# Kernel tuning notes

Hardware: AMD Instinct MI355X
Metric: run time of the kernel (lower is better)

The kernel has to match this reference:

```python
import jax, jax.numpy as jnp
import numpy as np

B, W, G, E, NI, K = 2048, 8192, 8, 128, 16, 15


def setup_inputs() -> dict:
    key = jax.random.key(0)
    ks = jax.random.split(key, 12)
    wavelengths_nm = jnp.linspace(300.0, 400.0, W, dtype=jnp.float32)
    # Rayleigh optical depth (Hansen & Travis style approximation), AMF=1 column
    lam_um = wavelengths_nm / 1000.0
    rayleigh_od = (0.008569 * lam_um ** -4
                   * (1.0 + 0.0113 * lam_um ** -2 + 0.00013 * lam_um ** -4)).astype(jnp.float32)
    return {
        "gas_columns": jax.random.uniform(ks[0], (B, G), jnp.float32),
        "instrument_ids": jax.random.randint(ks[1], (B,), 0, NI),
        "nuisance_latent": jax.random.normal(ks[2], (B, G), jnp.float32),
        "air_mass": 1.0 + 2.0 * jax.random.uniform(ks[3], (B,), jnp.float32),
        "wavelengths_nm": wavelengths_nm,
        "absorption": 0.1 * jax.random.uniform(ks[4], (G, W), jnp.float32),
        "continuum_basis": 0.05 * jax.random.normal(ks[5], (G + 1, W), jnp.float32),
        "rayleigh_od": rayleigh_od,
        "embed_table": jax.random.normal(ks[6], (NI, E), jnp.float32),
        "w1": jax.random.normal(ks[7], (E + G, 64), jnp.float32) / np.sqrt(E + G),
        "b1": jnp.zeros((64,), jnp.float32),
        "w2": jax.random.normal(ks[8], (64, 7), jnp.float32) / 8.0,
        "b2": jnp.zeros((7,), jnp.float32),
    }


def _gaussian_kernel(width_px, kernel_size):
    half = (kernel_size - 1) / 2
    pos = jnp.linspace(-half, half, kernel_size, dtype=width_px.dtype)  # [K]
    k = jnp.exp(-0.5 * (pos[None, :] / (width_px[:, None] + 1e-6)) ** 2)  # [B,K]
    return k / k.sum(axis=1, keepdims=True)


def _forward(gas_columns, nuisance_latent, air_mass, wavelengths_nm, absorption,
             continuum_basis, rayleigh_od, embed_table, w1, b1, w2, b2,
             instrument_ids):
    b = gas_columns.shape[0]
    am = air_mass[:, None]                                   # [B,1]
    scaled = gas_columns * am                                # [B,G]
    optical_depth = scaled @ absorption                      # [B,W]
    ones = jnp.ones((b, 1), gas_columns.dtype)
    continuum = jnp.concatenate([gas_columns, ones], axis=1) @ continuum_basis  # [B,W]
    differential = optical_depth + continuum + am * rayleigh_od[None, :]

    # nuisance MLP on [latent, embedding]
    embed = embed_table[instrument_ids]                      # [B,E]
    nin = jnp.concatenate([nuisance_latent, embed], axis=-1)
    h = jax.nn.gelu(nin @ w1 + b1, approximate=False)
    p = h @ w2 + b2                                          # [B,7]

    gain = jax.nn.softplus(p[:, 0]) + 0.001
    offset = p[:, 1]
    woff = 0.05 * jnp.tanh(p[:, 2])
    wscale = 1.0 + 0.005 * jnp.tanh(p[:, 3])
    lsf = jnp.clip(jax.nn.softplus(p[:, 4]) + 0.001, 0.2, 5.0)
    stray = jax.nn.sigmoid(p[:, 5]) * 0.05
    nonlin = 0.02 * jnp.tanh(p[:, 6])

    # per-sample wavelength shift/scale + linear resampling
    new_wl = wavelengths_nm[None, :] * wscale[:, None] + woff[:, None]  # [B,W]
    differential = jax.vmap(lambda wq, d: jnp.interp(wq, wavelengths_nm, d))(new_wl, differential)

    # per-sample Gaussian LSF convolution (replicate padding)
    kernel = _gaussian_kernel(lsf, K)                        # [B,K]
    pad = K // 2
    padded = jnp.pad(differential, ((0, 0), (pad, pad)), mode='edge')  # [B,W+K-1]
    n = differential.shape[1]
    convolved = sum(padded[:, k:k + n] * kernel[:, k:k + 1] for k in range(K))

    counts = jnp.exp(-convolved)
    post = gain[:, None] * counts + offset[:, None]
    total_nl = jnp.clip(nonlin, -0.04, 0.04)                 # instrument nonlinearity = 0
    nl_counts = post + total_nl[:, None] * post ** 2
    total_stray = jnp.clip(stray, 0.0, 0.2)                  # instrument stray = 0
    simulated = (1.0 - total_stray[:, None]) * nl_counts \
        + total_stray[:, None] * nl_counts.mean(axis=1, keepdims=True)
    return simulated


def reference(gas_columns, instrument_ids, nuisance_latent, air_mass,
              wavelengths_nm, absorption, continuum_basis, rayleigh_od,
              embed_table, w1, b1, w2, b2):
    return _forward(gas_columns, nuisance_latent, air_mass, wavelengths_nm,
                    absorption, continuum_basis, rayleigh_od, embed_table,
                    w1, b1, w2, b2, instrument_ids)
```

## Files before the change

### kernel.cpp

```cpp
#include <hip/hip_runtime.h>

#define W_ 8192
#define NBATCH 2048
#define TB 4
#define NT 512
#define CCH 1024
#define NCH 8
#define NSUB 16
#define RING 2048
#define RSTR 2052
#define IRW 1040

typedef unsigned short u16_t;
typedef _Float16 h2v __attribute__((ext_vector_type(2)));

__device__ __forceinline__ u16_t f2h(float x){ _Float16 h=(_Float16)x; return __builtin_bit_cast(u16_t,h); }
__device__ __forceinline__ float h2f(u16_t u){ return (float)__builtin_bit_cast(_Float16,u); }
__device__ __forceinline__ unsigned pk2(float a,float b){ return (unsigned)f2h(a)|((unsigned)f2h(b)<<16); }
__device__ __forceinline__ float dot2u(unsigned a,unsigned b,float c){
#if __has_builtin(__builtin_amdgcn_fdot2)
  return __builtin_amdgcn_fdot2(__builtin_bit_cast(h2v,a),__builtin_bit_cast(h2v,b),c,false);
#else
  h2v ha=__builtin_bit_cast(h2v,a), hb=__builtin_bit_cast(h2v,b);
  return c+(float)ha[0]*(float)hb[0]+(float)ha[1]*(float)hb[1];
#endif
}
__device__ __forceinline__ unsigned pkrtz(float a,float b){
#if __has_builtin(__builtin_amdgcn_cvt_pkrtz)
  return __builtin_bit_cast(unsigned, __builtin_amdgcn_cvt_pkrtz(a,b));
#else
  return pk2(a,b);
#endif
}
__device__ __forceinline__ float softplusf(float x){ return fmaxf(x,0.f)+log1pf(expf(-fabsf(x))); }

__global__ void doas_pack(const float* __restrict__ absn, const float* __restrict__ cbn,
                          const float* __restrict__ ray, unsigned* __restrict__ Tp){
  int w = blockIdx.x*256 + threadIdx.x;
  if (w >= W_) return;
  #pragma unroll
  for (int q=0;q<4;++q) Tp[q*W_+w]     = pk2(absn[(2*q)*W_+w], absn[(2*q+1)*W_+w]);
  #pragma unroll
  for (int q=0;q<4;++q) Tp[(4+q)*W_+w] = pk2(cbn[(2*q)*W_+w],  cbn[(2*q+1)*W_+w]);
  Tp[8*W_+w] = pk2(cbn[8*W_+w], ray[w]);
}

template<int PACKED>
__global__ __launch_bounds__(NT, 4)
void doas_main(const float* __restrict__ gas, const int* __restrict__ iid,
               const float* __restrict__ nuis, const float* __restrict__ air,
               const float* __restrict__ wl, const float* __restrict__ absn,
               const float* __restrict__ cbn, const float* __restrict__ ray,
               const float* __restrict__ emb, const float* __restrict__ w1,
               const float* __restrict__ b1, const float* __restrict__ w2,
               const float* __restrict__ b2, const unsigned* __restrict__ Tp,
               float* __restrict__ out)
{
  extern __shared__ char smem[];
  float* ringF = (float*)smem;
  float* irowS = (float*)(smem + TB*RSTR*4);
  float* hS    = (float*)(smem + TB*RSTR*4 + TB*IRW*4);
  float* pS    = hS + TB*64;
  float* scalS = pS + TB*8;
  float* wsumS = scalS + TB*32;

  const int tid = threadIdx.x;
  const int r0 = blockIdx.x * TB;

  if (tid < TB*64) {
    int rr = tid >> 6, j = tid & 63;
    int id = iid[r0 + rr];
    float acc = b1[j];
    const float* nrow = nuis + (size_t)(r0 + rr) * 8;
    #pragma unroll
    for (int i = 0; i < 8; ++i) acc = fmaf(nrow[i], w1[i*64 + j], acc);
    const float* erow = emb + (size_t)id * 128;
    for (int i = 0; i < 128; ++i) acc = fmaf(erow[i], w1[(8+i)*64 + j], acc);
    hS[rr*64 + j] = 0.5f * acc * (1.0f + erff(acc * 0.70710678118654752f));
  }
  __syncthreads();
  if (tid < TB*7) {
    int rr = tid / 7, k = tid % 7;
    float p = b2[k];
    for (int j = 0; j < 64; ++j) p = fmaf(hS[rr*64+j], w2[j*7+k], p);
    pS[rr*8+k] = p;
  }
  __syncthreads();
  if (tid < TB) {
    int rr = tid;
    float p0=pS[rr*8+0], p1=pS[rr*8+1], p2=pS[rr*8+2], p3=pS[rr*8+3],
          p4=pS[rr*8+4], p5=pS[rr*8+5], p6=pS[rr*8+6];
    float gainv = softplusf(p0) + 0.001f;
    float offv  = p1;
    float woffv = 0.05f * tanhf(p2);
    float wscv  = 1.0f + 0.005f * tanhf(p3);
    float lsf   = fminf(fmaxf(softplusf(p4) + 0.001f, 0.2f), 5.0f);
    float strv  = (1.0f/(1.0f+expf(-p5))) * 0.05f;
    float nlin  = 0.02f * tanhf(p6);
    nlin = fminf(fmaxf(nlin, -0.04f), 0.04f);
    strv = fminf(fmaxf(strv, 0.0f), 0.2f);
    float iw = 1.0f/(lsf + 1e-6f);
    float ks[15]; float ksum = 0.f;
    #pragma unroll
    for (int k2=0;k2<15;++k2){ float pp=(float)(k2-7)*iw; float e=expf(-0.5f*pp*pp); ks[k2]=e; ksum+=e; }
    float inv = 1.0f/ksum;
    float* sc = scalS + rr*32;
    #pragma unroll
    for (int k2=0;k2<15;++k2) sc[k2]=ks[k2]*inv;
    sc[15]=wscv; sc[16]=woffv; sc[17]=gainv; sc[18]=offv; sc[19]=nlin; sc[20]=strv;
    sc[22]=air[r0+rr];
    #pragma unroll
    for (int g=0; g<8; ++g) sc[23+g] = gas[(size_t)(r0+rr)*8+g];
  }
  __syncthreads();

  unsigned csg[TB][9];
  #pragma unroll
  for (int rr=0; rr<TB; ++rr){
    const float* scr = scalS + rr*32;
    float amr = scr[22];
    #pragma unroll
    for (int q=0;q<4;++q)
      csg[rr][q] = (unsigned)__builtin_amdgcn_readfirstlane(
          (int)pk2(scr[23+2*q]*amr, scr[23+2*q+1]*amr));
    #pragma unroll
    for (int q=0;q<4;++q)
      csg[rr][4+q] = (unsigned)__builtin_amdgcn_readfirstlane(
          (int)pk2(scr[23+2*q], scr[23+2*q+1]));
    csg[rr][8] = (unsigned)__builtin_amdgcn_readfirstlane((int)pk2(1.0f, amr));
  }

  const int r  = tid >> 7;
  const int wi = tid & 127;
  const float* sc = scalS + r*32;
  float kw[15];
  #pragma unroll
  for (int k2=0;k2<15;++k2) kw[k2]=sc[k2];
  const float wscale = sc[15], woff = sc[16], gainv = sc[17], offv = sc[18], nlin = sc[19];
  const float posoff = (300.0f*(wscale - 1.0f) + woff) * (8191.0f/100.0f);

  float* ring = ringF + r*RSTR;
  float* irow = irowS + r*IRW;

  auto do_diff = [&](int s){
    const int e = s*NT + tid;
    float a0=0.f, a1=0.f, a2=0.f, a3=0.f;
    if (PACKED){
      #pragma unroll
      for (int q=0;q<9;++q){
        unsigned d = Tp[q*W_ + e];
        a0 = dot2u(d, csg[0][q], a0);
        a1 = dot2u(d, csg[1][q], a1);
        a2 = dot2u(d, csg[2][q], a2);
        a3 = dot2u(d, csg[3][q], a3);
      }
    } else {
      float av[9][2];
      #pragma unroll
      for (int q=0;q<4;++q){ av[q][0]=absn[(2*q)*W_+e]; av[q][1]=absn[(2*q+1)*W_+e]; }
      #pragma unroll
      for (int q=0;q<4;++q){ av[4+q][0]=cbn[(2*q)*W_+e]; av[4+q][1]=cbn[(2*q+1)*W_+e]; }
      av[8][0]=cbn[8*W_+e]; av[8][1]=ray[e];
      float acc[TB]={0.f,0.f,0.f,0.f};
      #pragma unroll
      for (int rr=0;rr<TB;++rr){
        #pragma unroll
        for (int q=0;q<9;++q){
          acc[rr] = fmaf(h2f((u16_t)(csg[rr][q]&0xffffu)), av[q][0], acc[rr]);
          acc[rr] = fmaf(h2f((u16_t)(csg[rr][q]>>16)),     av[q][1], acc[rr]);
        }
      }
      a0=acc[0]; a1=acc[1]; a2=acc[2]; a3=acc[3];
    }
    const int p = e & (RING-1);
    ringF[0*RSTR+p]=a0; ringF[1*RSTR+p]=a1; ringF[2*RSTR+p]=a2; ringF[3*RSTR+p]=a3;
    if (p == 0){
      ringF[0*RSTR+RING]=a0; ringF[1*RSTR+RING]=a1;
      ringF[2*RSTR+RING]=a2; ringF[3*RSTR+RING]=a3;
    }
  };

  do_diff(0); do_diff(1); do_diff(2);

  float accsum = 0.f;
  unsigned nlp[NCH][4];

  #pragma unroll
  for (int c = 0; c < NCH; ++c) {
    const int cs = c * CCH;
    const bool eLo = (c == 0), eHi = (c == NCH-1);
    if (c >= 1) {
      if (2*c+1 < NSUB) do_diff(2*c+1);
      if (2*c+2 < NSUB) do_diff(2*c+2);
    }
    __syncthreads();
    #pragma unroll
    for (int it = 0; it < 5; ++it) {
      int jj = it*256 + 2*wi;
      if (jj < CCH + 14) {
        float v2[2];
        #pragma unroll
        for (int u=0; u<2; ++u){
          int j = cs - 7 + jj + u;
          int jc = j;
          if (eLo) jc = max(jc, 0);
          if (eHi) jc = min(jc, W_-1);
          float pos = fmaf((float)jc, wscale, posoff);
          if (eLo) pos = fmaxf(pos, 0.0f);
          if (eHi) pos = fminf(pos, 8191.0f);
          int i0 = (int)pos;
          if (eHi) i0 = min(i0, W_-2);
          float fr = pos - (float)i0;
          int p = i0 & (RING-1);
          float d0 = ring[p], d1 = ring[p+1];
          v2[u] = fmaf(fr, d1-d0, d0);
        }
        *(float2*)(irow + jj) = make_float2(v2[0], v2[1]);
      }
    }
    __syncthreads();
    {
      const int b0 = 8*wi;
      const float4* qp = (const float4*)(irow + b0);
      float4 A=qp[0], B=qp[1], C=qp[2], D=qp[3], E=qp[4], F=qp[5];
      float wr[24] = {A.x,A.y,A.z,A.w, B.x,B.y,B.z,B.w, C.x,C.y,C.z,C.w,
                      D.x,D.y,D.z,D.w, E.x,E.y,E.z,E.w, F.x,F.y,F.z,F.w};
      float nlv[8];
      #pragma unroll
      for (int j=0;j<8;++j){
        float cv = 0.f;
        #pragma unroll
        for (int t=0;t<15;++t) cv = fmaf(wr[j+t], kw[t], cv);
        float counts = __expf(-cv);
        float post = fmaf(gainv, counts, offv);
        float v = fmaf(nlin*post, post, post);
        accsum += v;
        nlv[j] = v;
      }
      nlp[c][0] = pkrtz(nlv[0], nlv[1]);
      nlp[c][1] = pkrtz(nlv[2], nlv[3]);
      nlp[c][2] = pkrtz(nlv[4], nlv[5]);
      nlp[c][3] = pkrtz(nlv[6], nlv[7]);
    }
  }

  float s = accsum;
  #pragma unroll
  for (int off2 = 32; off2 >= 1; off2 >>= 1) s += __shfl_down(s, off2);
  if ((tid & 63) == 0) wsumS[tid >> 6] = s;
  __syncthreads();
  if (tid < TB) scalS[tid*32 + 21] = (wsumS[2*tid] + wsumS[2*tid+1]) * (1.0f/8192.0f);
  __syncthreads();

  {
    const float strv = sc[20];
    const float meanv = sc[21];
    const float aa = 1.0f - strv;
    const float bb = strv * meanv;
    float* orow = out + (size_t)(r0 + r) * W_;
    #pragma unroll
    for (int c = 0; c < NCH; ++c) {
      unsigned u0 = nlp[c][0], u1 = nlp[c][1], u2 = nlp[c][2], u3 = nlp[c][3];
      float4 o0, o1;
      o0.x = fmaf(aa, h2f((u16_t)(u0 & 0xffffu)), bb);
      o0.y = fmaf(aa, h2f((u16_t)(u0 >> 16)),     bb);
      o0.z = fmaf(aa, h2f((u16_t)(u1 & 0xffffu)), bb);
      o0.w = fmaf(aa, h2f((u16_t)(u1 >> 16)),     bb);
      o1.x = fmaf(aa, h2f((u16_t)(u2 & 0xffffu)), bb);
      o1.y = fmaf(aa, h2f((u16_t)(u2 >> 16)),     bb);
      o1.z = fmaf(aa, h2f((u16_t)(u3 & 0xffffu)), bb);
      o1.w = fmaf(aa, h2f((u16_t)(u3 >> 16)),     bb);
      float* dst = orow + c*CCH + 8*wi;
      *(float4*)(dst)     = o0;
      *(float4*)(dst + 4) = o1;
    }
  }
}

extern "C" void kernel_launch(void* const* d_in, const int* in_sizes, int n_in,
                              void* d_out, int out_size, void* d_ws, size_t ws_size,
                              hipStream_t stream) {
  const float* gas  = (const float*)d_in[0];
  const int*   iid  = (const int*)d_in[1];
  const float* nuis = (const float*)d_in[2];
  const float* air  = (const float*)d_in[3];
  const float* wl   = (const float*)d_in[4];
  const float* absn = (const float*)d_in[5];
  const float* cbn  = (const float*)d_in[6];
  const float* ray  = (const float*)d_in[7];
  const float* emb  = (const float*)d_in[8];
  const float* w1   = (const float*)d_in[9];
  const float* b1   = (const float*)d_in[10];
  const float* w2   = (const float*)d_in[11];
  const float* b2   = (const float*)d_in[12];
  float* out = (float*)d_out;
  (void)in_sizes; (void)n_in; (void)out_size; (void)wl;

  const size_t ldsBytes = (size_t)TB*RSTR*4 + (size_t)TB*IRW*4
                        + (size_t)TB*64*4 + (size_t)TB*8*4 + (size_t)TB*32*4 + (NT/64)*4;
  const size_t packBytes = (size_t)9 * W_ * 4;

  if (ws_size >= packBytes) {
    unsigned* Tp = (unsigned*)d_ws;
    hipLaunchKernelGGL(doas_pack, dim3(W_/256), dim3(256), 0, stream, absn, cbn, ray, Tp);
    hipFuncSetAttribute(reinterpret_cast<const void*>(&doas_main<1>),
                        hipFuncAttributeMaxDynamicSharedMemorySize, (int)ldsBytes);
    hipLaunchKernelGGL((doas_main<1>), dim3(NBATCH/TB), dim3(NT), ldsBytes, stream,
                       gas, iid, nuis, air, wl, absn, cbn, ray, emb, w1, b1, w2, b2, Tp, out);
  } else {
    hipFuncSetAttribute(reinterpret_cast<const void*>(&doas_main<0>),
                        hipFuncAttributeMaxDynamicSharedMemorySize, (int)ldsBytes);
    hipLaunchKernelGGL((doas_main<0>), dim3(NBATCH/TB), dim3(NT), ldsBytes, stream,
                       gas, iid, nuis, air, wl, absn, cbn, ray, emb, w1, b1, w2, b2,
                       (const unsigned*)nullptr, out);
  }
}
```

Measured before the change: 57.55 us.

## Halve rows per block and interleave differential loads with convolution compute

Each block now handles 2 rows with 256 threads instead of 4 rows with 512, so there are twice as many blocks. The loads for the next differential sub-chunks are issued before the convolution's arithmetic and their dot products and ring stores are done afterwards, so global latency is hidden behind the exp/FMA work. The interpolated-row buffer in shared memory gets an XOR swizzle to reduce bank conflicts on the float4 reads. The cost is more registers held across the loop from the prefetched data, and the reduction and row-count logic now depends on the changed TB and NT.

```diff
diff --git a/kernel.cpp b/kernel.cpp
--- a/kernel.cpp
+++ b/kernel.cpp
@@ -2,11 +2,12 @@
 
 #define W_ 8192
 #define NBATCH 2048
-#define TB 4
-#define NT 512
+#define TB 2
+#define NT 256
 #define CCH 1024
 #define NCH 8
-#define NSUB 16
+#define SUBE 256
+#define NSUB 32
 #define RING 2048
 #define RSTR 2052
 #define IRW 1040
@@ -142,45 +143,48 @@
   float* ring = ringF + r*RSTR;
   float* irow = irowS + r*IRW;
 
-  auto do_diff = [&](int s){
-    const int e = s*NT + tid;
-    float a0=0.f, a1=0.f, a2=0.f, a3=0.f;
-    if (PACKED){
+  auto diff_load = [&](int s, unsigned* d){
+    const int e = s*SUBE + tid;
+    #pragma unroll
+    for (int q=0;q<9;++q) d[q] = Tp[q*W_ + e];
+  };
+  auto diff_store = [&](int s, const unsigned* d){
+    float a0=0.f, a1=0.f;
+    #pragma unroll
+    for (int q=0;q<9;++q){ a0 = dot2u(d[q], csg[0][q], a0); a1 = dot2u(d[q], csg[1][q], a1); }
+    const int p = (s*SUBE + tid) & (RING-1);
+    ringF[p] = a0; ringF[RSTR + p] = a1;
+    if (p == 0){ ringF[RING] = a0; ringF[RSTR + RING] = a1; }
+  };
+  auto diff_full = [&](int s){
+    const int e = s*SUBE + tid;
+    float av[9][2];
+    #pragma unroll
+    for (int q=0;q<4;++q){ av[q][0]=absn[(2*q)*W_+e]; av[q][1]=absn[(2*q+1)*W_+e]; }
+    #pragma unroll
+    for (int q=0;q<4;++q){ av[4+q][0]=cbn[(2*q)*W_+e]; av[4+q][1]=cbn[(2*q+1)*W_+e]; }
+    av[8][0]=cbn[8*W_+e]; av[8][1]=ray[e];
+    float acc[TB]={0.f,0.f};
+    #pragma unroll
+    for (int rr=0;rr<TB;++rr){
       #pragma unroll
       for (int q=0;q<9;++q){
-        unsigned d = Tp[q*W_ + e];
-        a0 = dot2u(d, csg[0][q], a0);
-        a1 = dot2u(d, csg[1][q], a1);
-        a2 = dot2u(d, csg[2][q], a2);
-        a3 = dot2u(d, csg[3][q], a3);
+        acc[rr] = fmaf(h2f((u16_t)(csg[rr][q]&0xffffu)), av[q][0], acc[rr]);
+        acc[rr] = fmaf(h2f((u16_t)(csg[rr][q]>>16)),     av[q][1], acc[rr]);
       }
-    } else {
-      float av[9][2];
-      #pragma unroll
-      for (int q=0;q<4;++q){ av[q][0]=absn[(2*q)*W_+e]; av[q][1]=absn[(2*q+1)*W_+e]; }
-      #pragma unroll
-      for (int q=0;q<4;++q){ av[4+q][0]=cbn[(2*q)*W_+e]; av[4+q][1]=cbn[(2*q+1)*W_+e]; }
-      av[8][0]=cbn[8*W_+e]; av[8][1]=ray[e];
-      float acc[TB]={0.f,0.f,0.f,0.f};
-      #pragma unroll
-      for (int rr=0;rr<TB;++rr){
-        #pragma unroll
-        for (int q=0;q<9;++q){
-          acc[rr] = fmaf(h2f((u16_t)(csg[rr][q]&0xffffu)), av[q][0], acc[rr]);
-          acc[rr] = fmaf(h2f((u16_t)(csg[rr][q]>>16)),     av[q][1], acc[rr]);
-        }
-      }
-      a0=acc[0]; a1=acc[1]; a2=acc[2]; a3=acc[3];
     }
     const int p = e & (RING-1);
-    ringF[0*RSTR+p]=a0; ringF[1*RSTR+p]=a1; ringF[2*RSTR+p]=a2; ringF[3*RSTR+p]=a3;
-    if (p == 0){
-      ringF[0*RSTR+RING]=a0; ringF[1*RSTR+RING]=a1;
-      ringF[2*RSTR+RING]=a2; ringF[3*RSTR+RING]=a3;
-    }
+    ringF[p] = acc[0]; ringF[RSTR + p] = acc[1];
+    if (p == 0){ ringF[RING] = acc[0]; ringF[RSTR + RING] = acc[1]; }
   };
 
-  do_diff(0); do_diff(1); do_diff(2);
+  if (PACKED){
+    unsigned d0p[9], d1p[9], d2p[9], d3p[9], d4p[9];
+    diff_load(0,d0p); diff_load(1,d1p); diff_load(2,d2p); diff_load(3,d3p); diff_load(4,d4p);
+    diff_store(0,d0p); diff_store(1,d1p); diff_store(2,d2p); diff_store(3,d3p); diff_store(4,d4p);
+  } else {
+    diff_full(0); diff_full(1); diff_full(2); diff_full(3); diff_full(4);
+  }
 
   float accsum = 0.f;
   unsigned nlp[NCH][4];
@@ -189,10 +193,6 @@
   for (int c = 0; c < NCH; ++c) {
     const int cs = c * CCH;
     const bool eLo = (c == 0), eHi = (c == NCH-1);
-    if (c >= 1) {
-      if (2*c+1 < NSUB) do_diff(2*c+1);
-      if (2*c+2 < NSUB) do_diff(2*c+2);
-    }
     __syncthreads();
     #pragma unroll
     for (int it = 0; it < 5; ++it) {
@@ -215,33 +215,71 @@
           float d0 = ring[p], d1 = ring[p+1];
           v2[u] = fmaf(fr, d1-d0, d0);
         }
-        *(float2*)(irow + jj) = make_float2(v2[0], v2[1]);
+        int uu = jj >> 2;
+        int su = uu ^ ((uu >> 3) & 7);
+        *(float2*)(irow + su*4 + (jj & 3)) = make_float2(v2[0], v2[1]);
       }
     }
     __syncthreads();
-    {
-      const int b0 = 8*wi;
-      const float4* qp = (const float4*)(irow + b0);
-      float4 A=qp[0], B=qp[1], C=qp[2], D=qp[3], E=qp[4], F=qp[5];
-      float wr[24] = {A.x,A.y,A.z,A.w, B.x,B.y,B.z,B.w, C.x,C.y,C.z,C.w,
-                      D.x,D.y,D.z,D.w, E.x,E.y,E.z,E.w, F.x,F.y,F.z,F.w};
-      float nlv[8];
+    const int sA = 4*c+5, sB = 4*c+6, sC = 4*c+7, sD = 4*c+8;
+    unsigned dA[9], dB[9];
+    if (PACKED){
+      if (sA < NSUB) diff_load(sA, dA);
+      if (sB < NSUB) diff_load(sB, dB);
+    }
+    float wr[24];
+    #pragma unroll
+    for (int k=0;k<6;++k){
+      int m = 2*wi + k;
+      int sm = m ^ ((m >> 3) & 7);
+      float4 t = *(const float4*)(irow + sm*4);
+      wr[4*k]=t.x; wr[4*k+1]=t.y; wr[4*k+2]=t.z; wr[4*k+3]=t.w;
+    }
+    float nlv[8];
+    #pragma unroll
+    for (int j=0;j<4;++j){
+      float cv = 0.f;
       #pragma unroll
-      for (int j=0;j<8;++j){
-        float cv = 0.f;
-        #pragma unroll
-        for (int t=0;t<15;++t) cv = fmaf(wr[j+t], kw[t], cv);
-        float counts = __expf(-cv);
-        float post = fmaf(gainv, counts, offv);
-        float v = fmaf(nlin*post, post, post);
-        accsum += v;
-        nlv[j] = v;
-      }
-      nlp[c][0] = pkrtz(nlv[0], nlv[1]);
-      nlp[c][1] = pkrtz(nlv[2], nlv[3]);
-      nlp[c][2] = pkrtz(nlv[4], nlv[5]);
-      nlp[c][3] = pkrtz(nlv[6], nlv[7]);
-    }
+      for (int t=0;t<15;++t) cv = fmaf(wr[j+t], kw[t], cv);
+      float counts = __expf(-cv);
+      float post = fmaf(gainv, counts, offv);
+      float v = fmaf(nlin*post, post, post);
+      accsum += v;
+      nlv[j] = v;
+    }
+    if (PACKED){
+      if (sA < NSUB) diff_store(sA, dA);
+      if (sB < NSUB) diff_store(sB, dB);
+    }
+    unsigned dC[9], dD[9];
+    if (PACKED){
+      if (sC < NSUB) diff_load(sC, dC);
+      if (sD < NSUB) diff_load(sD, dD);
+    }
+    #pragma unroll
+    for (int j=4;j<8;++j){
+      float cv = 0.f;
+      #pragma unroll
+      for (int t=0;t<15;++t) cv = fmaf(wr[j+t], kw[t], cv);
+      float counts = __expf(-cv);
+      float post = fmaf(gainv, counts, offv);
+      float v = fmaf(nlin*post, post, post);
+      accsum += v;
+      nlv[j] = v;
+    }
+    if (PACKED){
+      if (sC < NSUB) diff_store(sC, dC);
+      if (sD < NSUB) diff_store(sD, dD);
+    } else {
+      if (sA < NSUB) diff_full(sA);
+      if (sB < NSUB) diff_full(sB);
+      if (sC < NSUB) diff_full(sC);
+      if (sD < NSUB) diff_full(sD);
+    }
+    nlp[c][0] = pkrtz(nlv[0], nlv[1]);
+    nlp[c][1] = pkrtz(nlv[2], nlv[3]);
+    nlp[c][2] = pkrtz(nlv[4], nlv[5]);
+    nlp[c][3] = pkrtz(nlv[6], nlv[7]);
   }
 
   float s = accsum;
```

Measured after the change: 99.69 us. +73.2%, slower.
